# Kernel optimization log

Measured on AMD Instinct MI355X. Metric: run time of the kernel, lower is better.

The kernel has to match this reference:

```python
import jax, jax.numpy as jnp
import numpy as np

HIDDEN = 512
MEM = 512
COMM = 512
N = 8192


def setup_inputs() -> dict:
    key = jax.random.key(0)
    ks = jax.random.split(key, 8)
    in_dim = HIDDEN + MEM
    s = 1.0 / np.sqrt(in_dim)
    return {
        "u": jax.random.normal(ks[0], (N, HIDDEN), dtype=jnp.float32),
        "z": jax.random.normal(ks[1], (N, MEM), dtype=jnp.float32),
        # torch Linear weights have shape (out, in); biases init to 0 per _init_weights
        "Wk": jax.random.normal(ks[2], (COMM, in_dim), dtype=jnp.float32) * s,
        "bk": jnp.zeros((COMM,), dtype=jnp.float32),
        "Wv": jax.random.normal(ks[3], (COMM, in_dim), dtype=jnp.float32) * s,
        "bv": jnp.zeros((COMM,), dtype=jnp.float32),
        "Wq": jax.random.normal(ks[4], (COMM, in_dim), dtype=jnp.float32) * s,
        "bq": jnp.zeros((COMM,), dtype=jnp.float32),
    }


def reference(u, z, Wk, bk, Wv, bv, Wq, bq):
    n = u.shape[0]
    scale = jnp.sqrt(jnp.asarray(Wk.shape[0], dtype=u.dtype))
    s = jnp.concatenate([u, z], axis=-1)              # (N, in_dim)
    keys = s @ Wk.T + bk                              # (N, C)
    values = s @ Wv.T + bv                            # (N, C)
    queries = s @ Wq.T + bq                           # (N, C)
    scores = (queries @ keys.T) / scale               # (N, N)
    eye = jnp.eye(n, dtype=bool)
    scores = jnp.where(eye, -jnp.inf, scores)         # self-mask
    comm_attn = jax.nn.softmax(scores, axis=-1)
    comm_attn = jnp.nan_to_num(comm_attn, nan=0.0)
    m_bar = comm_attn @ values                        # (N, C)
    return (m_bar, comm_attn)
```

## Files before the change

### kernel.cpp

```cpp
#include <hip/hip_runtime.h>
#include <hip/hip_bf16.h>
#include <stdint.h>

#define N_TOK 8192
#define IN_DIM 1024
#define CDIM 512
#define NW 1536

typedef short bf16x8 __attribute__((ext_vector_type(8)));
typedef float f32x4 __attribute__((ext_vector_type(4)));

__device__ __forceinline__ unsigned short f2bf(float f) {
  union { float f; unsigned int u; } x; x.f = f;
  unsigned int u = x.u;
  u += 0x7fffu + ((u >> 16) & 1u);
  return (unsigned short)(u >> 16);
}
__device__ __forceinline__ float bf2f(unsigned short us) {
  union { unsigned int u; float f; } x; x.u = ((unsigned int)us) << 16;
  return x.f;
}

#define GLD16(g, l) __builtin_amdgcn_global_load_lds( \
    (const __attribute__((address_space(1))) void*)(g), \
    (__attribute__((address_space(3))) void*)(l), 16, 0, 0)

__global__ __launch_bounds__(256) void k_convert(
    const float* __restrict__ u, const float* __restrict__ z,
    const float* __restrict__ wk, const float* __restrict__ wv,
    const float* __restrict__ wq,
    ushort* __restrict__ Sb, ushort* __restrict__ Wb) {
  const int S4 = N_TOK * IN_DIM / 4;
  const int W4 = NW * IN_DIM / 4;
  const int total = S4 + W4;
  for (int e = blockIdx.x * blockDim.x + threadIdx.x; e < total;
       e += gridDim.x * blockDim.x) {
    float4 v; ushort* dst;
    if (e < S4) {
      int idx = e << 2; int row = idx >> 10; int col = idx & 1023;
      const float* src = (col < 512) ? (u + row * 512 + col)
                                     : (z + row * 512 + (col - 512));
      v = *(const float4*)src;
      dst = Sb + idx;
    } else {
      int idx = (e - S4) << 2; int row = idx >> 10; int col = idx & 1023;
      const float* base = (row < 512) ? wk : (row < 1024 ? wv : wq);
      v = *(const float4*)(base + (size_t)(row & 511) * 1024 + col);
      dst = Wb + idx;
    }
    ushort4 o;
    o.x = f2bf(v.x); o.y = f2bf(v.y); o.z = f2bf(v.z); o.w = f2bf(v.w);
    *(ushort4*)dst = o;
  }
}

__global__ __launch_bounds__(256) void k_kvq(
    const ushort* __restrict__ Sb, const ushort* __restrict__ Wb,
    const float* __restrict__ bk, const float* __restrict__ bv,
    const float* __restrict__ bq,
    ushort* __restrict__ Kb, ushort* __restrict__ Qb, ushort* __restrict__ VT) {
  __shared__ __align__(16) ushort As[128 * 64];
  __shared__ __align__(16) ushort Bs[128 * 64];
  const int tid = threadIdx.x, lane = tid & 63, w = tid >> 6;
  const int wr = w >> 1, wc = w & 1;
  const int tm = blockIdx.x, tn = blockIdx.y;

  f32x4 acc[4][4];
#pragma unroll
  for (int m = 0; m < 4; m++)
#pragma unroll
    for (int n = 0; n < 4; n++) acc[m][n] = (f32x4){0.f, 0.f, 0.f, 0.f};

  const ushort* ga0 = Sb + (size_t)tm * 128 * IN_DIM;
  const ushort* gb0 = Wb + (size_t)tn * 128 * IN_DIM;

  for (int k0 = 0; k0 < IN_DIM; k0 += 64) {
#pragma unroll
    for (int i = 0; i < 4; i++) {
      int ce = i * 256 + tid;
      int row = ce >> 3, c8 = (ce & 7) << 3;
      GLD16(ga0 + (size_t)row * IN_DIM + k0 + c8, As + ce * 8);
      GLD16(gb0 + (size_t)row * IN_DIM + k0 + c8, Bs + ce * 8);
    }
    __syncthreads();
#pragma unroll
    for (int kb = 0; kb < 2; kb++) {
      bf16x8 af[4], bfr[4];
#pragma unroll
      for (int m = 0; m < 4; m++)
        af[m] = *(const bf16x8*)(As + (wr * 64 + m * 16 + (lane & 15)) * 64 +
                                 kb * 32 + ((lane >> 4) << 3));
#pragma unroll
      for (int n = 0; n < 4; n++)
        bfr[n] = *(const bf16x8*)(Bs + (wc * 64 + n * 16 + (lane & 15)) * 64 +
                                  kb * 32 + ((lane >> 4) << 3));
#pragma unroll
      for (int m = 0; m < 4; m++)
#pragma unroll
        for (int n = 0; n < 4; n++)
          acc[m][n] = __builtin_amdgcn_mfma_f32_16x16x32_bf16(af[m], bfr[n],
                                                              acc[m][n], 0, 0, 0);
    }
    __syncthreads();
  }

  const int region = tn >> 2;
  const int colr = (tn & 3) * 128 + wc * 64;
  const int rbase = tm * 128 + wr * 64;
  const float* bias = (region == 0) ? bk : (region == 1 ? bv : bq);
  if (region == 1) {
#pragma unroll
    for (int m = 0; m < 4; m++) {
      int r0 = rbase + m * 16 + ((lane >> 4) << 2);
#pragma unroll
      for (int n = 0; n < 4; n++) {
        int c = colr + n * 16 + (lane & 15);
        float b = bias[c];
        ushort4 pk;
        pk.x = f2bf(acc[m][n][0] + b);
        pk.y = f2bf(acc[m][n][1] + b);
        pk.z = f2bf(acc[m][n][2] + b);
        pk.w = f2bf(acc[m][n][3] + b);
        *(ushort4*)(VT + (size_t)c * N_TOK + r0) = pk;
      }
    }
  } else {
    ushort* O = (region == 0) ? Kb : Qb;
#pragma unroll
    for (int m = 0; m < 4; m++) {
      int r0 = rbase + m * 16 + ((lane >> 4) << 2);
#pragma unroll
      for (int n = 0; n < 4; n++) {
        int c = colr + n * 16 + (lane & 15);
        float b = bias[c];
#pragma unroll
        for (int rg = 0; rg < 4; rg++)
          O[(size_t)(r0 + rg) * CDIM + c] = f2bf(acc[m][n][rg] + b);
      }
    }
  }
}

__global__ __launch_bounds__(256) void k_scores(
    const ushort* __restrict__ Qb, const ushort* __restrict__ Kb,
    ushort* __restrict__ E, float* __restrict__ rowpart) {
  __shared__ __align__(16) ushort As[128 * 64];
  __shared__ __align__(16) ushort Bs[128 * 64];
  __shared__ float sums[256];
  const int tid = threadIdx.x, lane = tid & 63, w = tid >> 6;
  const int wr = w >> 1, wc = w & 1;
  const int bid = blockIdx.x;
  const int swz = (bid & 7) * 512 + (bid >> 3);
  const int tm = swz & 63, tn = swz >> 6;

  f32x4 acc[4][4];
#pragma unroll
  for (int m = 0; m < 4; m++)
#pragma unroll
    for (int n = 0; n < 4; n++) acc[m][n] = (f32x4){0.f, 0.f, 0.f, 0.f};

  const ushort* ga0 = Qb + (size_t)tm * 128 * CDIM;
  const ushort* gb0 = Kb + (size_t)tn * 128 * CDIM;

  for (int k0 = 0; k0 < CDIM; k0 += 64) {
#pragma unroll
    for (int i = 0; i < 4; i++) {
      int ce = i * 256 + tid;
      int row = ce >> 3, c8 = (ce & 7) << 3;
      GLD16(ga0 + (size_t)row * CDIM + k0 + c8, As + ce * 8);
      GLD16(gb0 + (size_t)row * CDIM + k0 + c8, Bs + ce * 8);
    }
    __syncthreads();
#pragma unroll
    for (int kb = 0; kb < 2; kb++) {
      bf16x8 af[4], bfr[4];
#pragma unroll
      for (int m = 0; m < 4; m++)
        af[m] = *(const bf16x8*)(As + (wr * 64 + m * 16 + (lane & 15)) * 64 +
                                 kb * 32 + ((lane >> 4) << 3));
#pragma unroll
      for (int n = 0; n < 4; n++)
        bfr[n] = *(const bf16x8*)(Bs + (wc * 64 + n * 16 + (lane & 15)) * 64 +
                                  kb * 32 + ((lane >> 4) << 3));
#pragma unroll
      for (int m = 0; m < 4; m++)
#pragma unroll
        for (int n = 0; n < 4; n++)
          acc[m][n] = __builtin_amdgcn_mfma_f32_16x16x32_bf16(af[m], bfr[n],
                                                              acc[m][n], 0, 0, 0);
    }
    __syncthreads();
  }

  const float scale = 0.044194173824159216f;
  float rs[4][4];
#pragma unroll
  for (int m = 0; m < 4; m++)
#pragma unroll
    for (int rg = 0; rg < 4; rg++) rs[m][rg] = 0.f;

#pragma unroll
  for (int m = 0; m < 4; m++) {
    int grow_b = tm * 128 + wr * 64 + m * 16 + ((lane >> 4) << 2);
#pragma unroll
    for (int n = 0; n < 4; n++) {
      int gcol = tn * 128 + wc * 64 + n * 16 + (lane & 15);
#pragma unroll
      for (int rg = 0; rg < 4; rg++) {
        int grow = grow_b + rg;
        float ev = (grow == gcol) ? 0.0f : __expf(acc[m][n][rg] * scale);
        unsigned short evb = f2bf(ev);
        E[(size_t)grow * N_TOK + gcol] = evb;
        rs[m][rg] += bf2f(evb);
      }
    }
  }
#pragma unroll
  for (int m = 0; m < 4; m++)
#pragma unroll
    for (int rg = 0; rg < 4; rg++) {
      float s = rs[m][rg];
      s += __shfl_xor(s, 1);
      s += __shfl_xor(s, 2);
      s += __shfl_xor(s, 4);
      s += __shfl_xor(s, 8);
      rs[m][rg] = s;
    }
  if ((lane & 15) == 0) {
#pragma unroll
    for (int m = 0; m < 4; m++)
#pragma unroll
      for (int rg = 0; rg < 4; rg++)
        sums[wc * 128 + wr * 64 + m * 16 + ((lane >> 4) << 2) + rg] = rs[m][rg];
  }
  __syncthreads();
  if (tid < 128)
    rowpart[(size_t)(tm * 128 + tid) * 64 + tn] = sums[tid] + sums[128 + tid];
}

__global__ __launch_bounds__(256) void k_rcp(const float* __restrict__ rowpart,
                                             float* __restrict__ rcp_l) {
  int row = blockIdx.x * blockDim.x + threadIdx.x;
  if (row < N_TOK) {
    const float4* p = (const float4*)(rowpart + (size_t)row * 64);
    float s = 0.f;
#pragma unroll
    for (int i = 0; i < 16; i++) {
      float4 v = p[i];
      s += v.x + v.y + v.z + v.w;
    }
    rcp_l[row] = 1.0f / s;
  }
}

__global__ __launch_bounds__(256) void k_pv(
    const ushort* __restrict__ E, const ushort* __restrict__ VT,
    float* __restrict__ part0, float* __restrict__ part1,
    float* __restrict__ part2, float* __restrict__ part3) {
  __shared__ __align__(16) ushort As[128 * 64];
  __shared__ __align__(16) ushort Bs[128 * 64];
  const int tid = threadIdx.x, lane = tid & 63, w = tid >> 6;
  const int wr = w >> 1, wc = w & 1;
  const int tn = blockIdx.x, kz = blockIdx.y, tm = blockIdx.z;
  const int kbase = kz << 11;

  f32x4 acc[4][4];
#pragma unroll
  for (int m = 0; m < 4; m++)
#pragma unroll
    for (int n = 0; n < 4; n++) acc[m][n] = (f32x4){0.f, 0.f, 0.f, 0.f};

  const ushort* ga0 = E + (size_t)tm * 128 * N_TOK;
  const ushort* gb0 = VT + (size_t)tn * 128 * N_TOK;
  const int sx = lane & 7;

  for (int k0 = kbase; k0 < kbase + 2048; k0 += 64) {
#pragma unroll
    for (int i = 0; i < 4; i++) {
      int ce = i * 256 + tid;
      int row = ce >> 3;
      int c8 = ((ce & 7) ^ (row & 7)) << 3;
      GLD16(ga0 + (size_t)row * N_TOK + k0 + c8, As + ce * 8);
      GLD16(gb0 + (size_t)row * N_TOK + k0 + c8, Bs + ce * 8);
    }
    __syncthreads();
#pragma unroll
    for (int kb = 0; kb < 2; kb++) {
      const int chunk = ((kb * 4 + (lane >> 4)) ^ sx) << 3;
      bf16x8 af[4], bfr[4];
#pragma unroll
      for (int m = 0; m < 4; m++)
        af[m] = *(const bf16x8*)(As + (wr * 64 + m * 16 + (lane & 15)) * 64 +
                                 chunk);
#pragma unroll
      for (int n = 0; n < 4; n++)
        bfr[n] = *(const bf16x8*)(Bs + (wc * 64 + n * 16 + (lane & 15)) * 64 +
                                  chunk);
#pragma unroll
      for (int m = 0; m < 4; m++)
#pragma unroll
        for (int n = 0; n < 4; n++)
          acc[m][n] = __builtin_amdgcn_mfma_f32_16x16x32_bf16(af[m], bfr[n],
                                                              acc[m][n], 0, 0, 0);
    }
    __syncthreads();
  }

  float* P = (kz == 0) ? part0 : (kz == 1) ? part1 : (kz == 2) ? part2 : part3;
#pragma unroll
  for (int m = 0; m < 4; m++) {
    int r0 = tm * 128 + wr * 64 + m * 16 + ((lane >> 4) << 2);
#pragma unroll
    for (int n = 0; n < 4; n++) {
      int c = tn * 128 + wc * 64 + n * 16 + (lane & 15);
#pragma unroll
      for (int rg = 0; rg < 4; rg++)
        P[(size_t)(r0 + rg) * CDIM + c] = acc[m][n][rg];
    }
  }
}

__global__ __launch_bounds__(256) void k_reduce4(
    float* __restrict__ p0, const float* __restrict__ p1,
    const float* __restrict__ p2, const float* __restrict__ p3,
    const float* __restrict__ rcp_l) {
  int idx4 = blockIdx.x * blockDim.x + threadIdx.x;
  const int T4 = N_TOK * CDIM / 4;
  if (idx4 < T4) {
    int row = idx4 >> 7;
    float rl = rcp_l[row];
    float4 a = ((const float4*)p0)[idx4];
    float4 b = ((const float4*)p1)[idx4];
    float4 c = ((const float4*)p2)[idx4];
    float4 d = ((const float4*)p3)[idx4];
    float4 o;
    o.x = (a.x + b.x + c.x + d.x) * rl;
    o.y = (a.y + b.y + c.y + d.y) * rl;
    o.z = (a.z + b.z + c.z + d.z) * rl;
    o.w = (a.w + b.w + c.w + d.w) * rl;
    ((float4*)p0)[idx4] = o;
  }
}

__global__ __launch_bounds__(256) void k_norm(
    const ushort* __restrict__ E, float* __restrict__ attn,
    const float* __restrict__ rcp_l, int row0, int nrows) {
  const int units = nrows << 10;
  for (int uidx = blockIdx.x * blockDim.x + threadIdx.x; uidx < units;
       uidx += gridDim.x * blockDim.x) {
    int row = row0 + (uidx >> 10);
    int c8 = (uidx & 1023) << 3;
    const float rl = rcp_l[row];
    uint4 ev = *(const uint4*)(E + ((size_t)row << 13) + c8);
    float4 o0, o1;
    o0.x = bf2f((unsigned short)(ev.x & 0xffffu)) * rl;
    o0.y = bf2f((unsigned short)(ev.x >> 16)) * rl;
    o0.z = bf2f((unsigned short)(ev.y & 0xffffu)) * rl;
    o0.w = bf2f((unsigned short)(ev.y >> 16)) * rl;
    o1.x = bf2f((unsigned short)(ev.z & 0xffffu)) * rl;
    o1.y = bf2f((unsigned short)(ev.z >> 16)) * rl;
    o1.z = bf2f((unsigned short)(ev.w & 0xffffu)) * rl;
    o1.w = bf2f((unsigned short)(ev.w >> 16)) * rl;
    float* op = attn + ((size_t)row << 13) + c8;
    *(float4*)op = o0;
    *(float4*)(op + 4) = o1;
  }
}

__global__ __launch_bounds__(256) void k_lastrow(
    const ushort* __restrict__ E, float* __restrict__ attn,
    const float* __restrict__ rcp_l) {
  const int row = N_TOK - 1;
  const int t = threadIdx.x;
  const float rl = rcp_l[row];
  const uint4* src = (const uint4*)(E + ((size_t)row << 13)) + t * 4;
  uint4 rr[4] = {src[0], src[1], src[2], src[3]};
  __syncthreads();
  float* dst = attn + ((size_t)row << 13) + t * 32;
#pragma unroll
  for (int q = 0; q < 4; q++) {
    float4 o0, o1;
    o0.x = bf2f((unsigned short)(rr[q].x & 0xffffu)) * rl;
    o0.y = bf2f((unsigned short)(rr[q].x >> 16)) * rl;
    o0.z = bf2f((unsigned short)(rr[q].y & 0xffffu)) * rl;
    o0.w = bf2f((unsigned short)(rr[q].y >> 16)) * rl;
    o1.x = bf2f((unsigned short)(rr[q].z & 0xffffu)) * rl;
    o1.y = bf2f((unsigned short)(rr[q].z >> 16)) * rl;
    o1.z = bf2f((unsigned short)(rr[q].w & 0xffffu)) * rl;
    o1.w = bf2f((unsigned short)(rr[q].w >> 16)) * rl;
    *(float4*)(dst + q * 8) = o0;
    *(float4*)(dst + q * 8 + 4) = o1;
  }
}

extern "C" void kernel_launch(void* const* d_in, const int* in_sizes, int n_in,
                              void* d_out, int out_size, void* d_ws,
                              size_t ws_size, hipStream_t stream) {
  const float* u  = (const float*)d_in[0];
  const float* z  = (const float*)d_in[1];
  const float* Wk = (const float*)d_in[2];
  const float* bk = (const float*)d_in[3];
  const float* Wv = (const float*)d_in[4];
  const float* bv = (const float*)d_in[5];
  const float* Wq = (const float*)d_in[6];
  const float* bq = (const float*)d_in[7];

  float* mbar = (float*)d_out;
  float* attn = (float*)d_out + (size_t)N_TOK * CDIM;

  char* ws = (char*)d_ws;
  ushort* Kb      = (ushort*)(ws + 0);
  ushort* Qb      = (ushort*)(ws + 8388608);
  ushort* VT      = (ushort*)(ws + 16777216);
  float*  rcp_l   = (float*)(ws + 25165824);
  float*  rowpart = (float*)(ws + 25198592);
  ushort* Sb      = (ushort*)(ws + 27295744);
  ushort* Wb      = (ushort*)(ws + 44072960);
  const size_t E_WS_OFF = 27295744;
  const size_t REQ = E_WS_OFF + 134217728;
  const bool ws_mode = (ws_size >= REQ);
  ushort* E = ws_mode ? (ushort*)(ws + E_WS_OFF)
                      : (ushort*)((char*)attn + 134217728);
  float* part1 = attn;
  float* part2 = attn + (size_t)N_TOK * CDIM;
  float* part3 = attn + (size_t)2 * N_TOK * CDIM;

  k_convert<<<dim3(2048), dim3(256), 0, stream>>>(u, z, Wk, Wv, Wq, Sb, Wb);
  k_kvq<<<dim3(64, 12), dim3(256), 0, stream>>>(Sb, Wb, bk, bv, bq, Kb, Qb, VT);
  k_scores<<<dim3(4096), dim3(256), 0, stream>>>(Qb, Kb, E, rowpart);
  k_rcp<<<dim3(32), dim3(256), 0, stream>>>(rowpart, rcp_l);
  k_pv<<<dim3(4, 4, 64), dim3(256), 0, stream>>>(E, VT, mbar, part1, part2,
                                                 part3);
  k_reduce4<<<dim3(4096), dim3(256), 0, stream>>>(mbar, part1, part2, part3,
                                                  rcp_l);

  if (ws_mode) {
    k_norm<<<dim3(2048), dim3(256), 0, stream>>>(E, attn, rcp_l, 0, N_TOK);
  } else {
    static const int ph[] = {0, 4096, 6144, 7168, 7680, 7936, 8064, 8128,
                             8160, 8176, 8184, 8188, 8190, 8191};
    for (int p = 0; p + 1 < (int)(sizeof(ph) / sizeof(ph[0])); ++p) {
      int a = ph[p], b = ph[p + 1];
      int units = (b - a) << 10;
      int blocks = (units + 255) / 256;
      if (blocks > 2048) blocks = 2048;
      k_norm<<<dim3(blocks), dim3(256), 0, stream>>>(E, attn, rcp_l, a, b - a);
    }
    k_lastrow<<<dim3(1), dim3(256), 0, stream>>>(E, attn, rcp_l);
  }
}
```

Before: 391.5 us.

## Fuse PV GEMM with attention normalization in one launch, halve split-K

The PV matmul and the bf16-to-fp32 normalization of the attention matrix now run as a single launch: the first 512 blocks compute PV tiles and the remaining 1536 blocks stream E into the normalized attn output. The goal is to overlap the compute-bound GEMM with the bandwidth-bound 256MB write. Split-K drops from 4 to 2, so fewer partial buffers are written and reduced. The second partial now lives in workspace (aliasing the Kb/Qb region, which is dead by then) rather than in attn, which the normalization is writing at the same time. The block-index remap groups tm tiles for better L2 reuse. The fused blocks compete for CUs, and with fewer PV blocks each one runs longer.

```diff
diff --git a/kernel.cpp b/kernel.cpp
--- a/kernel.cpp
+++ b/kernel.cpp
@@ -253,16 +253,45 @@
   }
 }
 
-__global__ __launch_bounds__(256) void k_pv(
+__global__ __launch_bounds__(256) void k_pv_fused(
     const ushort* __restrict__ E, const ushort* __restrict__ VT,
-    float* __restrict__ part0, float* __restrict__ part1,
-    float* __restrict__ part2, float* __restrict__ part3) {
+    const float* __restrict__ rcp_l, float* __restrict__ part0,
+    float* __restrict__ part1, float* __restrict__ attn) {
   __shared__ __align__(16) ushort As[128 * 64];
   __shared__ __align__(16) ushort Bs[128 * 64];
-  const int tid = threadIdx.x, lane = tid & 63, w = tid >> 6;
+  const int bid = blockIdx.x;
+  const int tid = threadIdx.x;
+
+  if (bid >= 512) {
+    const int units = N_TOK * 1024;
+    const int stride = 1536 * 256;
+    for (int uidx = (bid - 512) * 256 + tid; uidx < units; uidx += stride) {
+      int row = uidx >> 10;
+      int c8 = (uidx & 1023) << 3;
+      const float rl = rcp_l[row];
+      uint4 ev = *(const uint4*)(E + ((size_t)row << 13) + c8);
+      float4 o0, o1;
+      o0.x = bf2f((unsigned short)(ev.x & 0xffffu)) * rl;
+      o0.y = bf2f((unsigned short)(ev.x >> 16)) * rl;
+      o0.z = bf2f((unsigned short)(ev.y & 0xffffu)) * rl;
+      o0.w = bf2f((unsigned short)(ev.y >> 16)) * rl;
+      o1.x = bf2f((unsigned short)(ev.z & 0xffffu)) * rl;
+      o1.y = bf2f((unsigned short)(ev.z >> 16)) * rl;
+      o1.z = bf2f((unsigned short)(ev.w & 0xffffu)) * rl;
+      o1.w = bf2f((unsigned short)(ev.w >> 16)) * rl;
+      float* op = attn + ((size_t)row << 13) + c8;
+      *(float4*)op = o0;
+      *(float4*)(op + 4) = o1;
+    }
+    return;
+  }
+
+  const int lane = tid & 63, w = tid >> 6;
   const int wr = w >> 1, wc = w & 1;
-  const int tn = blockIdx.x, kz = blockIdx.y, tm = blockIdx.z;
-  const int kbase = kz << 11;
+  const int inner = (bid >> 3) & 7;
+  const int tn = inner & 3, kz = inner >> 2;
+  const int tm = ((bid >> 6) << 3) | (bid & 7);
+  const int kbase = kz << 12;
 
   f32x4 acc[4][4];
 #pragma unroll
@@ -274,7 +303,7 @@
   const ushort* gb0 = VT + (size_t)tn * 128 * N_TOK;
   const int sx = lane & 7;
 
-  for (int k0 = kbase; k0 < kbase + 2048; k0 += 64) {
+  for (int k0 = kbase; k0 < kbase + 4096; k0 += 64) {
 #pragma unroll
     for (int i = 0; i < 4; i++) {
       int ce = i * 256 + tid;
@@ -306,7 +335,7 @@
     __syncthreads();
   }
 
-  float* P = (kz == 0) ? part0 : (kz == 1) ? part1 : (kz == 2) ? part2 : part3;
+  float* P = kz ? part1 : part0;
 #pragma unroll
   for (int m = 0; m < 4; m++) {
     int r0 = tm * 128 + wr * 64 + m * 16 + ((lane >> 4) << 2);
@@ -320,9 +349,74 @@
   }
 }
 
-__global__ __launch_bounds__(256) void k_reduce4(
+__global__ __launch_bounds__(256) void k_pv(
+    const ushort* __restrict__ E, const ushort* __restrict__ VT,
+    float* __restrict__ part0, float* __restrict__ part1) {
+  __shared__ __align__(16) ushort As[128 * 64];
+  __shared__ __align__(16) ushort Bs[128 * 64];
+  const int tid = threadIdx.x, lane = tid & 63, w = tid >> 6;
+  const int wr = w >> 1, wc = w & 1;
+  const int tn = blockIdx.x, kz = blockIdx.y, tm = blockIdx.z;
+  const int kbase = kz << 12;
+
+  f32x4 acc[4][4];
+#pragma unroll
+  for (int m = 0; m < 4; m++)
+#pragma unroll
+    for (int n = 0; n < 4; n++) acc[m][n] = (f32x4){0.f, 0.f, 0.f, 0.f};
+
+  const ushort* ga0 = E + (size_t)tm * 128 * N_TOK;
+  const ushort* gb0 = VT + (size_t)tn * 128 * N_TOK;
+  const int sx = lane & 7;
+
+  for (int k0 = kbase; k0 < kbase + 4096; k0 += 64) {
+#pragma unroll
+    for (int i = 0; i < 4; i++) {
+      int ce = i * 256 + tid;
+      int row = ce >> 3;
+      int c8 = ((ce & 7) ^ (row & 7)) << 3;
+      GLD16(ga0 + (size_t)row * N_TOK + k0 + c8, As + ce * 8);
+      GLD16(gb0 + (size_t)row * N_TOK + k0 + c8, Bs + ce * 8);
+    }
+    __syncthreads();
+#pragma unroll
+    for (int kb = 0; kb < 2; kb++) {
+      const int chunk = ((kb * 4 + (lane >> 4)) ^ sx) << 3;
+      bf16x8 af[4], bfr[4];
+#pragma unroll
+      for (int m = 0; m < 4; m++)
+        af[m] = *(const bf16x8*)(As + (wr * 64 + m * 16 + (lane & 15)) * 64 +
+                                 chunk);
+#pragma unroll
+      for (int n = 0; n < 4; n++)
+        bfr[n] = *(const bf16x8*)(Bs + (wc * 64 + n * 16 + (lane & 15)) * 64 +
+                                  chunk);
+#pragma unroll
+      for (int m = 0; m < 4; m++)
+#pragma unroll
+        for (int n = 0; n < 4; n++)
+          acc[m][n] = __builtin_amdgcn_mfma_f32_16x16x32_bf16(af[m], bfr[n],
+                                                              acc[m][n], 0, 0, 0);
+    }
+    __syncthreads();
+  }
+
+  float* P = kz ? part1 : part0;
+#pragma unroll
+  for (int m = 0; m < 4; m++) {
+    int r0 = tm * 128 + wr * 64 + m * 16 + ((lane >> 4) << 2);
+#pragma unroll
+    for (int n = 0; n < 4; n++) {
+      int c = tn * 128 + wc * 64 + n * 16 + (lane & 15);
+#pragma unroll
+      for (int rg = 0; rg < 4; rg++)
+        P[(size_t)(r0 + rg) * CDIM + c] = acc[m][n][rg];
+    }
+  }
+}
+
+__global__ __launch_bounds__(256) void k_reduce2(
     float* __restrict__ p0, const float* __restrict__ p1,
-    const float* __restrict__ p2, const float* __restrict__ p3,
     const float* __restrict__ rcp_l) {
   int idx4 = blockIdx.x * blockDim.x + threadIdx.x;
   const int T4 = N_TOK * CDIM / 4;
@@ -331,13 +425,9 @@
     float rl = rcp_l[row];
     float4 a = ((const float4*)p0)[idx4];
     float4 b = ((const float4*)p1)[idx4];
-    float4 c = ((const float4*)p2)[idx4];
-    float4 d = ((const float4*)p3)[idx4];
     float4 o;
-    o.x = (a.x + b.x + c.x + d.x) * rl;
-    o.y = (a.y + b.y + c.y + d.y) * rl;
-    o.z = (a.z + b.z + c.z + d.z) * rl;
-    o.w = (a.w + b.w + c.w + d.w) * rl;
+    o.x = (a.x + b.x) * rl; o.y = (a.y + b.y) * rl;
+    o.z = (a.z + b.z) * rl; o.w = (a.w + b.w) * rl;
     ((float4*)p0)[idx4] = o;
   }
 }
@@ -416,27 +506,26 @@
   float*  rowpart = (float*)(ws + 25198592);
   ushort* Sb      = (ushort*)(ws + 27295744);
   ushort* Wb      = (ushort*)(ws + 44072960);
+  float*  part1ws = (float*)(ws + 0);
   const size_t E_WS_OFF = 27295744;
   const size_t REQ = E_WS_OFF + 134217728;
   const bool ws_mode = (ws_size >= REQ);
   ushort* E = ws_mode ? (ushort*)(ws + E_WS_OFF)
                       : (ushort*)((char*)attn + 134217728);
-  float* part1 = attn;
-  float* part2 = attn + (size_t)N_TOK * CDIM;
-  float* part3 = attn + (size_t)2 * N_TOK * CDIM;
 
   k_convert<<<dim3(2048), dim3(256), 0, stream>>>(u, z, Wk, Wv, Wq, Sb, Wb);
   k_kvq<<<dim3(64, 12), dim3(256), 0, stream>>>(Sb, Wb, bk, bv, bq, Kb, Qb, VT);
   k_scores<<<dim3(4096), dim3(256), 0, stream>>>(Qb, Kb, E, rowpart);
   k_rcp<<<dim3(32), dim3(256), 0, stream>>>(rowpart, rcp_l);
-  k_pv<<<dim3(4, 4, 64), dim3(256), 0, stream>>>(E, VT, mbar, part1, part2,
-                                                 part3);
-  k_reduce4<<<dim3(4096), dim3(256), 0, stream>>>(mbar, part1, part2, part3,
-                                                  rcp_l);
 
   if (ws_mode) {
-    k_norm<<<dim3(2048), dim3(256), 0, stream>>>(E, attn, rcp_l, 0, N_TOK);
+    k_pv_fused<<<dim3(2048), dim3(256), 0, stream>>>(E, VT, rcp_l, mbar,
+                                                     part1ws, attn);
+    k_reduce2<<<dim3(4096), dim3(256), 0, stream>>>(mbar, part1ws, rcp_l);
   } else {
+    float* part1 = attn;
+    k_pv<<<dim3(4, 2, 64), dim3(256), 0, stream>>>(E, VT, mbar, part1);
+    k_reduce2<<<dim3(4096), dim3(256), 0, stream>>>(mbar, part1, rcp_l);
     static const int ph[] = {0, 4096, 6144, 7168, 7680, 7936, 8064, 8128,
                              8160, 8176, 8184, 8188, 8190, 8191};
     for (int p = 0; p + 1 < (int)(sizeof(ph) / sizeof(ph[0])); ++p) {
```

After: 368.6 us, median of 2. 5.9% less time.
